# Performance work log

Measured on AMD Instinct MI355X. Metric: run time of the kernel, lower is better.

Reference implementation:

```python
import jax, jax.numpy as jnp
import numpy as np

K_V_DIM = 100
_SQRT_D = float(np.sqrt(K_V_DIM))


def _dk_layer(q, k, v, Wq, bq, Wk, n_unsqueeze):
    """One DKEncoder_layer: DK_text + DK_knowledge + DK_fusion (CokeBert attention).
    q: [B, q_dim]; k: [..., n, K_V_DIM]; v: [..., n, d_v].
    Attention over the last neighbor axis n.
    """
    # DK_text: linear + tanh + unsqueeze to broadcast against k
    q_i = jnp.tanh(q @ Wq.T + bq)                               # [B, D]
    q_i = q_i.reshape((q_i.shape[0],) + (1,) * n_unsqueeze + (K_V_DIM,))
    # DK_knowledge: bias-free linear on k
    k = k @ Wk.T
    # DK_fusion (CokeBert): scaled dot, mask zeros, leaky_relu+softmax, zero out fully-masked rows
    attn = (q_i * k).sum(-1) / _SQRT_D                          # [..., n]
    attn = jnp.where(attn == 0.0, -10000.0, attn)
    attn = jax.nn.softmax(jax.nn.leaky_relu(attn), axis=-1)
    n = attn.shape[-1]
    attn = jnp.where(attn == 1.0 / n, 0.0, attn)
    return jnp.einsum('...n,...nd->...d', attn, v)              # [..., d_v]


def setup_inputs() -> dict:
    key = jax.random.key(0)
    ks = jax.random.split(key, 12)
    B, S, E, N1, N2, D, Q = 8, 256, 256, 16, 16, K_V_DIM, 768
    return {
        "input_ent": jax.random.randint(ks[0], (B, S), 0, 2, dtype=jnp.int64),
        "q": jax.random.normal(ks[1], (B, S, Q), dtype=jnp.float32),
        "k1": jax.random.normal(ks[2], (B, E, N1, D), dtype=jnp.float32),
        "v1": jax.random.normal(ks[3], (B, E, N1, D), dtype=jnp.float32),
        "k2": jax.random.normal(ks[4], (B, E, N1, N2, D), dtype=jnp.float32),
        "v2": jax.random.normal(ks[5], (B, E, N1, N2, D), dtype=jnp.float32),
        # layers[0] has layer_no=2 (deepest), layers[1] has layer_no=1
        "Wq2": jax.random.normal(ks[6], (D, Q), dtype=jnp.float32) * 0.05,
        "bq2": jnp.zeros((D,), dtype=jnp.float32),
        "Wk2": jax.random.normal(ks[7], (D, D), dtype=jnp.float32) * 0.1,
        "Wq1": jax.random.normal(ks[8], (D, Q), dtype=jnp.float32) * 0.05,
        "bq1": jnp.zeros((D,), dtype=jnp.float32),
        "Wk1": jax.random.normal(ks[9], (D, D), dtype=jnp.float32) * 0.1,
    }


def reference(input_ent, q, k1, v1, k2, v2, Wq2, bq2, Wk2, Wq1, bq1, Wk1):
    q0 = q[:, 0, :]                                             # [B, Q]
    # layer 0 (layer_no=2): reduce innermost neighbor axis
    combined = _dk_layer(q0, k2, v2, Wq2, bq2, Wk2, 3)          # [B, E, N1, D]
    # layer 1 (layer_no=1): v = cat([v1, combined])
    v1c = jnp.concatenate([v1, combined], axis=-1)              # [B, E, N1, 2D]
    combined = _dk_layer(q0, k1, v1c, Wq1, bq1, Wk1, 2)         # [B, E, 2D]
    # scatter: i-th nonzero position of input_ent[b] receives combined[b, i]
    mask = input_ent != 0                                       # [B, S]
    rank = jnp.cumsum(mask.astype(jnp.int32), axis=1) - 1       # [B, S]
    rank = jnp.clip(rank, 0, combined.shape[1] - 1)
    gathered = jnp.take_along_axis(combined, rank[..., None], axis=1)  # [B, S, 2D]
    return jnp.where(mask[..., None], gathered, 0.0)
```

## Files before the change

### kernel.cpp

```cpp
#include <hip/hip_runtime.h>
#include <cstddef>
#include <cstdint>

#define BB 8
#define SS 256
#define EE 256
#define NN1 16
#define NN2 16
#define DD 100
#define QQ 768

__global__ __launch_bounds__(256) void prep_kernel(
    const float* __restrict__ q, const int* __restrict__ ent,
    const float* __restrict__ Wq2, const float* __restrict__ bq2, const float* __restrict__ Wk2,
    const float* __restrict__ Wq1, const float* __restrict__ bq1, const float* __restrict__ Wk1,
    float* __restrict__ qk2o, float* __restrict__ qk1o, int* __restrict__ rk)
{
    const int blk = blockIdx.x, t = threadIdx.x;
    if (blk < 16) {
        const int b = blk >> 1, layer = blk & 1;
        const float* Wq = layer ? Wq1 : Wq2;
        const float* bq = layer ? bq1 : bq2;
        const float* Wk = layer ? Wk1 : Wk2;
        float* qko      = layer ? qk1o : qk2o;
        __shared__ float s_q[QQ];
        __shared__ float s_qi[DD];
        for (int i = t; i < QQ; i += 256) s_q[i] = q[(size_t)b * SS * QQ + i];
        __syncthreads();
        const int r = t & 7;
        for (int d = t >> 3; d < DD; d += 32) {
            float acc = 0.f;
            for (int i = r; i < QQ; i += 8) acc += Wq[(size_t)d * QQ + i] * s_q[i];
            acc += __shfl_xor(acc, 1, 8);
            acc += __shfl_xor(acc, 2, 8);
            acc += __shfl_xor(acc, 4, 8);
            if (r == 0) s_qi[d] = tanhf(acc + bq[d]);
        }
        __syncthreads();
        if (t < DD) {
            float acc = 0.f;
            for (int d = 0; d < DD; ++d) acc += s_qi[d] * Wk[d * DD + t];
            qko[b * DD + t] = 0.1f * acc;
        }
    } else {
        const int b = blk - 16;
        __shared__ int s_m[SS];
        const int m = (ent[b * SS + t] != 0) ? 1 : 0;
        s_m[t] = m;
        __syncthreads();
        for (int off = 1; off < SS; off <<= 1) {
            const int add = (t >= off) ? s_m[t - off] : 0;
            __syncthreads();
            s_m[t] += add;
            __syncthreads();
        }
        int rank = s_m[t] - 1;
        rank = rank < 0 ? 0 : (rank > EE - 1 ? EE - 1 : rank);
        rk[b * SS + t] = m ? rank : -1;
    }
}

__global__ __launch_bounds__(256) void dk2_kernel(
    const float* __restrict__ k2, const float* __restrict__ v2,
    const float* __restrict__ qk2g, float* __restrict__ c2, int b0)
{
    const int blk = blockIdx.x;
    const int n1  = blk & 15;
    const int bbe = blk >> 4;
    const int b   = b0 + (bbe >> 8);
    const int t   = threadIdx.x;
    const int gi  = t >> 4;
    const int rr  = t & 15;

    __shared__ float s_logit[16];
    __shared__ float s_p[16];

    const size_t base = ((size_t)(((b << 8) | (bbe & 255)) * 16 + n1)) * (size_t)(NN2 * DD);

    const float* krow = k2 + base + gi * DD;
    const float* qk   = qk2g + b * DD;
    float acc = 0.f;
    #pragma unroll
    for (int j = 0; j < 7; ++j) {
        const int d = rr + 16 * j;
        if (d < DD) acc += krow[d] * qk[d];
    }
    acc += __shfl_xor(acc, 1, 16);
    acc += __shfl_xor(acc, 2, 16);
    acc += __shfl_xor(acc, 4, 16);
    acc += __shfl_xor(acc, 8, 16);
    if (rr == 0) {
        float lg = acc;
        if (lg == 0.0f) lg = -10000.0f;
        s_logit[gi] = lg >= 0.f ? lg : 0.01f * lg;
    }
    __syncthreads();

    float lg = s_logit[t & 15];
    float mx = lg;
    mx = fmaxf(mx, __shfl_xor(mx, 1, 16));
    mx = fmaxf(mx, __shfl_xor(mx, 2, 16));
    mx = fmaxf(mx, __shfl_xor(mx, 4, 16));
    mx = fmaxf(mx, __shfl_xor(mx, 8, 16));
    const float e = __expf(lg - mx);
    float sm = e;
    sm += __shfl_xor(sm, 1, 16);
    sm += __shfl_xor(sm, 2, 16);
    sm += __shfl_xor(sm, 4, 16);
    sm += __shfl_xor(sm, 8, 16);
    float p = e / sm;
    if (p == 0.0625f) p = 0.f;
    if (t < 16) s_p[t] = p;
    __syncthreads();

    if (t < DD) {
        const float* vb = v2 + base;
        float a = 0.f;
        #pragma unroll
        for (int n = 0; n < NN2; ++n) a += s_p[n] * vb[n * DD + t];
        c2[((size_t)bbe * NN1 + n1) * DD + t] = a;
    }
}

__global__ __launch_bounds__(256) void dk1_kernel(
    const float* __restrict__ k1, const float* __restrict__ v1,
    const float* __restrict__ c2, const float* __restrict__ qk1g,
    float* __restrict__ comb, int b0)
{
    const int bbe = blockIdx.x;
    const int b   = b0 + (bbe >> 8);
    const int be  = (b << 8) | (bbe & 255);
    const int t   = threadIdx.x;
    const int gi  = t >> 4;
    const int rr  = t & 15;

    __shared__ float s_logit[16];
    __shared__ float s_p[16];

    const size_t base = (size_t)be * (NN1 * DD);

    const float* krow = k1 + base + gi * DD;
    const float* qk   = qk1g + b * DD;
    float acc = 0.f;
    #pragma unroll
    for (int j = 0; j < 7; ++j) {
        const int d = rr + 16 * j;
        if (d < DD) acc += krow[d] * qk[d];
    }
    acc += __shfl_xor(acc, 1, 16);
    acc += __shfl_xor(acc, 2, 16);
    acc += __shfl_xor(acc, 4, 16);
    acc += __shfl_xor(acc, 8, 16);
    if (rr == 0) {
        float lg = acc;
        if (lg == 0.0f) lg = -10000.0f;
        s_logit[gi] = lg >= 0.f ? lg : 0.01f * lg;
    }
    __syncthreads();

    float lg = s_logit[t & 15];
    float mx = lg;
    mx = fmaxf(mx, __shfl_xor(mx, 1, 16));
    mx = fmaxf(mx, __shfl_xor(mx, 2, 16));
    mx = fmaxf(mx, __shfl_xor(mx, 4, 16));
    mx = fmaxf(mx, __shfl_xor(mx, 8, 16));
    const float e = __expf(lg - mx);
    float sm = e;
    sm += __shfl_xor(sm, 1, 16);
    sm += __shfl_xor(sm, 2, 16);
    sm += __shfl_xor(sm, 4, 16);
    sm += __shfl_xor(sm, 8, 16);
    float p = e / sm;
    if (p == 0.0625f) p = 0.f;
    if (t < 16) s_p[t] = p;
    __syncthreads();

    if (t < 2 * DD) {
        float a = 0.f;
        if (t < DD) {
            const float* vb = v1 + base;
            #pragma unroll
            for (int n = 0; n < NN1; ++n) a += s_p[n] * vb[n * DD + t];
        } else {
            const int d = t - DD;
            const float* cb = c2 + (size_t)bbe * (NN1 * DD);
            #pragma unroll
            for (int n = 0; n < NN1; ++n) a += s_p[n] * cb[n * DD + d];
        }
        comb[(size_t)be * (2 * DD) + t] = a;
    }
}

__global__ __launch_bounds__(64) void gather_kernel(
    const float* __restrict__ comb, const int* __restrict__ rk, float* __restrict__ out)
{
    const int bs = blockIdx.x;
    const int b  = bs >> 8;
    const int t  = threadIdx.x;
    const int r  = rk[bs];
    float* o = out + (size_t)bs * (2 * DD);
    if (r < 0) {
        for (int d = t; d < 2 * DD; d += 64) o[d] = 0.f;
    } else {
        const float* src = comb + (size_t)(b * EE + r) * (2 * DD);
        for (int d = t; d < 2 * DD; d += 64) o[d] = src[d];
    }
}

extern "C" void kernel_launch(void* const* d_in, const int* in_sizes, int n_in,
                              void* d_out, int out_size, void* d_ws, size_t ws_size,
                              hipStream_t stream)
{
    const int*   ent = (const int*)d_in[0];
    const float* q   = (const float*)d_in[1];
    const float* k1  = (const float*)d_in[2];
    const float* v1  = (const float*)d_in[3];
    const float* k2  = (const float*)d_in[4];
    const float* v2  = (const float*)d_in[5];
    const float* Wq2 = (const float*)d_in[6];
    const float* bq2 = (const float*)d_in[7];
    const float* Wk2 = (const float*)d_in[8];
    const float* Wq1 = (const float*)d_in[9];
    const float* bq1 = (const float*)d_in[10];
    const float* Wk1 = (const float*)d_in[11];
    float* out = (float*)d_out;

    float* ws   = (float*)d_ws;
    float* qk2  = ws;
    float* qk1  = ws + 1024;
    int*   rk   = (int*)(ws + 2048);
    float* comb = ws + 4096;
    float* c2   = ws + 4096 + 409600;

    const size_t fixed = 4096 + 409600;
    const size_t perb  = (size_t)EE * NN1 * DD;
    size_t wsf = ws_size / sizeof(float);
    int kb = (wsf > fixed) ? (int)((wsf - fixed) / perb) : 1;
    if (kb < 1) kb = 1;
    if (kb > BB) kb = BB;

    prep_kernel<<<24, 256, 0, stream>>>(q, ent, Wq2, bq2, Wk2, Wq1, bq1, Wk1, qk2, qk1, rk);
    for (int b0 = 0; b0 < BB; b0 += kb) {
        const int nb = (BB - b0 < kb) ? (BB - b0) : kb;
        dk2_kernel<<<nb * EE * NN1, 256, 0, stream>>>(k2, v2, qk2, c2, b0);
        dk1_kernel<<<nb * EE,       256, 0, stream>>>(k1, v1, c2, qk1, comb, b0);
    }
    gather_kernel<<<BB * SS, 64, 0, stream>>>(comb, rk, out);
}
```

Measured before the change: 159.7 us.

## Vectorize k/v loads with float4 and process two neighbor groups per block

The dk2 kernel now handles two N1 slices per block, loading the whole k and v tiles with coalesced float4 reads, staging v in shared memory, and computing partial dot products per float4 chunk before a reduction. dk1 is restructured the same way, also staging the c2 intermediate, and the softmax weights are broadcast through shuffles instead of shared memory and a barrier. The prep projection uses float4 dot products. The aim is fewer, wider memory transactions on the bandwidth-bound k2/v2 stream and half as many blocks, at the cost of more shared memory per block and possibly lower occupancy.

```diff
diff --git a/kernel.cpp b/kernel.cpp
--- a/kernel.cpp
+++ b/kernel.cpp
@@ -9,6 +9,10 @@
 #define NN2 16
 #define DD 100
 #define QQ 768
+
+__device__ __forceinline__ float dot4(float4 a, float4 b) {
+    return a.x * b.x + a.y * b.y + a.z * b.z + a.w * b.w;
+}
 
 __global__ __launch_bounds__(256) void prep_kernel(
     const float* __restrict__ q, const int* __restrict__ ent,
@@ -27,10 +31,12 @@
         __shared__ float s_qi[DD];
         for (int i = t; i < QQ; i += 256) s_q[i] = q[(size_t)b * SS * QQ + i];
         __syncthreads();
+        const float4* sq4 = (const float4*)s_q;
         const int r = t & 7;
         for (int d = t >> 3; d < DD; d += 32) {
+            const float4* wq4 = (const float4*)(Wq + (size_t)d * QQ);
             float acc = 0.f;
-            for (int i = r; i < QQ; i += 8) acc += Wq[(size_t)d * QQ + i] * s_q[i];
+            for (int c = r; c < QQ / 4; c += 8) acc += dot4(wq4[c], sq4[c]);
             acc += __shfl_xor(acc, 1, 8);
             acc += __shfl_xor(acc, 2, 8);
             acc += __shfl_xor(acc, 4, 8);
@@ -62,37 +68,116 @@
 
 __global__ __launch_bounds__(256) void dk2_kernel(
     const float* __restrict__ k2, const float* __restrict__ v2,
-    const float* __restrict__ qk2g, float* __restrict__ c2, int b0)
+    const float* __restrict__ qk2g, float* __restrict__ c2o, int b0)
 {
     const int blk = blockIdx.x;
-    const int n1  = blk & 15;
-    const int bbe = blk >> 4;
+    const int pi  = blk & 7;
+    const int bbe = blk >> 3;
     const int b   = b0 + (bbe >> 8);
+    const int be  = (b << 8) | (bbe & 255);
     const int t   = threadIdx.x;
-    const int gi  = t >> 4;
-    const int rr  = t & 15;
-
+
+    __shared__ float s_part[800];
+    __shared__ float s_v[3200];
+    __shared__ float s_logit[32];
+    float4* sv4 = (float4*)s_v;
+
+    const size_t tb = ((size_t)(be * NN1 + pi * 2)) * 400;
+    const float4* kt  = (const float4*)k2 + tb;
+    const float4* vt  = (const float4*)v2 + tb;
+    const float4* qkb = (const float4*)qk2g + b * 25;
+
+    const int i0 = t, i1 = t + 256, i2 = t + 512, i3 = t + 768;
+    float4 ka0 = kt[i0], ka1 = kt[i1], ka2 = kt[i2];
+    float4 va0 = vt[i0], va1 = vt[i1], va2 = vt[i2];
+    float4 ka3, va3;
+    if (t < 32) { ka3 = kt[i3]; va3 = vt[i3]; }
+    const int c0 = i0 % 25, c1 = i1 % 25, c2 = i2 % 25, c3 = i3 % 25;
+    const float4 q0 = qkb[c0], q1 = qkb[c1], q2 = qkb[c2], q3 = qkb[c3];
+
+    s_part[i0] = dot4(ka0, q0); sv4[i0] = va0;
+    s_part[i1] = dot4(ka1, q1); sv4[i1] = va1;
+    s_part[i2] = dot4(ka2, q2); sv4[i2] = va2;
+    if (t < 32) { s_part[i3] = dot4(ka3, q3); sv4[i3] = va3; }
+    __syncthreads();
+
+    if (t < 32) {
+        float acc = 0.f;
+        #pragma unroll
+        for (int c = 0; c < 25; ++c) acc += s_part[t * 25 + c];
+        if (acc == 0.0f) acc = -10000.0f;
+        s_logit[t] = acc >= 0.f ? acc : 0.01f * acc;
+    }
+    __syncthreads();
+
+    const int half = t >> 7;
+    float lg = s_logit[half * 16 + (t & 15)];
+    float mx = lg;
+    mx = fmaxf(mx, __shfl_xor(mx, 1, 16));
+    mx = fmaxf(mx, __shfl_xor(mx, 2, 16));
+    mx = fmaxf(mx, __shfl_xor(mx, 4, 16));
+    mx = fmaxf(mx, __shfl_xor(mx, 8, 16));
+    const float e = __expf(lg - mx);
+    float sm = e;
+    sm += __shfl_xor(sm, 1, 16);
+    sm += __shfl_xor(sm, 2, 16);
+    sm += __shfl_xor(sm, 4, 16);
+    sm += __shfl_xor(sm, 8, 16);
+    float p = e / sm;
+    if (p == 0.0625f) p = 0.f;
+    float pn[16];
+    #pragma unroll
+    for (int n = 0; n < 16; ++n) pn[n] = __shfl(p, n, 16);
+
+    const int lt = t & 127;
+    if (lt < DD) {
+        const float* vb = s_v + half * 1600;
+        float a = 0.f;
+        #pragma unroll
+        for (int n = 0; n < NN2; ++n) a += pn[n] * vb[n * DD + lt];
+        c2o[((size_t)bbe * NN1 + pi * 2 + half) * DD + lt] = a;
+    }
+}
+
+__global__ __launch_bounds__(256) void dk1_kernel(
+    const float* __restrict__ k1, const float* __restrict__ v1,
+    const float* __restrict__ c2i, const float* __restrict__ qk1g,
+    float* __restrict__ comb, int b0)
+{
+    const int bbe = blockIdx.x;
+    const int b   = b0 + (bbe >> 8);
+    const int be  = (b << 8) | (bbe & 255);
+    const int t   = threadIdx.x;
+
+    __shared__ float s_part[400];
+    __shared__ float s_v[1600];
+    __shared__ float s_c[1600];
     __shared__ float s_logit[16];
-    __shared__ float s_p[16];
-
-    const size_t base = ((size_t)(((b << 8) | (bbe & 255)) * 16 + n1)) * (size_t)(NN2 * DD);
-
-    const float* krow = k2 + base + gi * DD;
-    const float* qk   = qk2g + b * DD;
-    float acc = 0.f;
-    #pragma unroll
-    for (int j = 0; j < 7; ++j) {
-        const int d = rr + 16 * j;
-        if (d < DD) acc += krow[d] * qk[d];
-    }
-    acc += __shfl_xor(acc, 1, 16);
-    acc += __shfl_xor(acc, 2, 16);
-    acc += __shfl_xor(acc, 4, 16);
-    acc += __shfl_xor(acc, 8, 16);
-    if (rr == 0) {
-        float lg = acc;
-        if (lg == 0.0f) lg = -10000.0f;
-        s_logit[gi] = lg >= 0.f ? lg : 0.01f * lg;
+    float4* sv4 = (float4*)s_v;
+    float4* sc4 = (float4*)s_c;
+
+    const float4* kt  = (const float4*)k1 + (size_t)be * 400;
+    const float4* vt  = (const float4*)v1 + (size_t)be * 400;
+    const float4* ct  = (const float4*)c2i + (size_t)bbe * 400;
+    const float4* qkb = (const float4*)qk1g + b * 25;
+
+    const int i0 = t, i1 = t + 256;
+    float4 ka0 = kt[i0], va0 = vt[i0], ca0 = ct[i0];
+    float4 ka1, va1, ca1;
+    if (t < 144) { ka1 = kt[i1]; va1 = vt[i1]; ca1 = ct[i1]; }
+    const int c0 = i0 % 25, c1 = i1 % 25;
+    const float4 q0 = qkb[c0], q1 = qkb[c1];
+
+    s_part[i0] = dot4(ka0, q0); sv4[i0] = va0; sc4[i0] = ca0;
+    if (t < 144) { s_part[i1] = dot4(ka1, q1); sv4[i1] = va1; sc4[i1] = ca1; }
+    __syncthreads();
+
+    if (t < 16) {
+        float acc = 0.f;
+        #pragma unroll
+        for (int c = 0; c < 25; ++c) acc += s_part[t * 25 + c];
+        if (acc == 0.0f) acc = -10000.0f;
+        s_logit[t] = acc >= 0.f ? acc : 0.01f * acc;
     }
     __syncthreads();
 
@@ -110,82 +195,19 @@
     sm += __shfl_xor(sm, 8, 16);
     float p = e / sm;
     if (p == 0.0625f) p = 0.f;
-    if (t < 16) s_p[t] = p;
-    __syncthreads();
-
-    if (t < DD) {
-        const float* vb = v2 + base;
-        float a = 0.f;
-        #pragma unroll
-        for (int n = 0; n < NN2; ++n) a += s_p[n] * vb[n * DD + t];
-        c2[((size_t)bbe * NN1 + n1) * DD + t] = a;
-    }
-}
-
-__global__ __launch_bounds__(256) void dk1_kernel(
-    const float* __restrict__ k1, const float* __restrict__ v1,
-    const float* __restrict__ c2, const float* __restrict__ qk1g,
-    float* __restrict__ comb, int b0)
-{
-    const int bbe = blockIdx.x;
-    const int b   = b0 + (bbe >> 8);
-    const int be  = (b << 8) | (bbe & 255);
-    const int t   = threadIdx.x;
-    const int gi  = t >> 4;
-    const int rr  = t & 15;
-
-    __shared__ float s_logit[16];
-    __shared__ float s_p[16];
-
-    const size_t base = (size_t)be * (NN1 * DD);
-
-    const float* krow = k1 + base + gi * DD;
-    const float* qk   = qk1g + b * DD;
-    float acc = 0.f;
+    float pn[16];
     #pragma unroll
-    for (int j = 0; j < 7; ++j) {
-        const int d = rr + 16 * j;
-        if (d < DD) acc += krow[d] * qk[d];
-    }
-    acc += __shfl_xor(acc, 1, 16);
-    acc += __shfl_xor(acc, 2, 16);
-    acc += __shfl_xor(acc, 4, 16);
-    acc += __shfl_xor(acc, 8, 16);
-    if (rr == 0) {
-        float lg = acc;
-        if (lg == 0.0f) lg = -10000.0f;
-        s_logit[gi] = lg >= 0.f ? lg : 0.01f * lg;
-    }
-    __syncthreads();
-
-    float lg = s_logit[t & 15];
-    float mx = lg;
-    mx = fmaxf(mx, __shfl_xor(mx, 1, 16));
-    mx = fmaxf(mx, __shfl_xor(mx, 2, 16));
-    mx = fmaxf(mx, __shfl_xor(mx, 4, 16));
-    mx = fmaxf(mx, __shfl_xor(mx, 8, 16));
-    const float e = __expf(lg - mx);
-    float sm = e;
-    sm += __shfl_xor(sm, 1, 16);
-    sm += __shfl_xor(sm, 2, 16);
-    sm += __shfl_xor(sm, 4, 16);
-    sm += __shfl_xor(sm, 8, 16);
-    float p = e / sm;
-    if (p == 0.0625f) p = 0.f;
-    if (t < 16) s_p[t] = p;
-    __syncthreads();
+    for (int n = 0; n < 16; ++n) pn[n] = __shfl(p, n, 16);
 
     if (t < 2 * DD) {
         float a = 0.f;
         if (t < DD) {
-            const float* vb = v1 + base;
             #pragma unroll
-            for (int n = 0; n < NN1; ++n) a += s_p[n] * vb[n * DD + t];
+            for (int n = 0; n < NN1; ++n) a += pn[n] * s_v[n * DD + t];
         } else {
             const int d = t - DD;
-            const float* cb = c2 + (size_t)bbe * (NN1 * DD);
             #pragma unroll
-            for (int n = 0; n < NN1; ++n) a += s_p[n] * cb[n * DD + d];
+            for (int n = 0; n < NN1; ++n) a += pn[n] * s_c[n * DD + d];
         }
         comb[(size_t)be * (2 * DD) + t] = a;
     }
@@ -242,8 +264,8 @@
     prep_kernel<<<24, 256, 0, stream>>>(q, ent, Wq2, bq2, Wk2, Wq1, bq1, Wk1, qk2, qk1, rk);
     for (int b0 = 0; b0 < BB; b0 += kb) {
         const int nb = (BB - b0 < kb) ? (BB - b0) : kb;
-        dk2_kernel<<<nb * EE * NN1, 256, 0, stream>>>(k2, v2, qk2, c2, b0);
-        dk1_kernel<<<nb * EE,       256, 0, stream>>>(k1, v1, c2, qk1, comb, b0);
+        dk2_kernel<<<nb * EE * 8, 256, 0, stream>>>(k2, v2, qk2, c2, b0);
+        dk1_kernel<<<nb * EE,     256, 0, stream>>>(k1, v1, c2, qk1, comb, b0);
     }
     gather_kernel<<<BB * SS, 64, 0, stream>>>(comb, rk, out);
 }
```

Result: faster. 146.5 us (-8.3%).
